# Performance work log

Measured on AMD Instinct MI355X. Metric: run time of the kernel, lower is better.

Reference implementation:

```python
import jax, jax.numpy as jnp
import numpy as np

NUM_USER = 60000
NUM_ITEM = 40000
DIM_C = 64
NUM_EDGES = 1_000_000
NUM_ROUTING = 3
ALPHA_THRESHOLD = 0.02
REATTN = True
NEG_SLOPE = 0.2  # PyG GAT default leaky-relu slope
EPS = 1e-16


def l2norm(x):
    # F.normalize(x): L2 along last dim with eps clamp
    return x / jnp.clip(jnp.linalg.norm(x, axis=-1, keepdims=True), 1e-12, None)


def seg_softmax(s, seg, n):
    # numerically stable softmax over edges grouped by target node
    m = jax.ops.segment_max(s, seg, num_segments=n)
    e = jnp.exp(s - m[seg])
    den = jax.ops.segment_sum(e, seg, num_segments=n)
    return e / (den[seg] + EPS)


def setup_inputs() -> dict:
    key = jax.random.key(0)
    ks = jax.random.split(key, 6)
    xav = (2.0 / (NUM_USER + DIM_C)) ** 0.5  # xavier_normal_ scale for preference
    features = jax.random.normal(ks[0], (NUM_ITEM, DIM_C), jnp.float32)
    features2 = jax.random.normal(ks[1], (NUM_ITEM, DIM_C), jnp.float32)
    features3 = jax.random.normal(ks[2], (NUM_ITEM, DIM_C), jnp.float32)
    preference = jax.random.normal(ks[3], (NUM_USER, DIM_C), jnp.float32) * xav
    users = jax.random.randint(ks[4], (NUM_EDGES,), 0, NUM_USER, dtype=jnp.int32)
    items = jax.random.randint(ks[5], (NUM_EDGES,), 0, NUM_ITEM, dtype=jnp.int32) + NUM_USER
    edge_index = jnp.stack([users, items], axis=0)  # [2, E] user -> item (item ids offset by num_user)
    return {"features": features, "features2": features2, "features3": features3,
            "preference": preference, "edge_index": edge_index}


def reference(features, features2, features3, preference, edge_index):
    n = NUM_USER + NUM_ITEM
    inv_sqrt_d = 1.0 / np.sqrt(DIM_C).astype(np.float32)

    pref = l2norm(preference)
    x = jnp.concatenate([pref, l2norm(features)], axis=0)   # [N, d]
    y = jnp.concatenate([pref, l2norm(features2)], axis=0)
    z = jnp.concatenate([pref, l2norm(features3)], axis=0)

    # symmetrize: edge_index = cat(edge_index, edge_index[[1,0]])
    ei = jnp.concatenate([edge_index, edge_index[::-1]], axis=1)  # [2, 2E]
    src, dst = ei[0], ei[1]  # message flows src(j) -> dst(i)

    # --- conv_embed_1: multimodal GAT with thresholding + re-attention ---
    s = ((x[dst] * x[src]).sum(-1)
         + (y[dst] * y[src]).sum(-1)
         + (z[dst] * z[src]).sum(-1)) * inv_sqrt_d          # [2E]
    alpha = seg_softmax(jax.nn.leaky_relu(s, NEG_SLOPE), dst, n)
    alpha_t = jnp.where(alpha > ALPHA_THRESHOLD, alpha, 0.0)
    if REATTN:
        den = jax.ops.segment_sum(alpha_t, dst, num_segments=n)
        alpha_t = alpha_t / (den[dst] + EPS)
    x_hat = jax.ops.segment_sum(x[src] * alpha_t[:, None], dst, num_segments=n)
    x = l2norm(x + x_hat)

    # --- routing iterations with plain dot-product GAT (conv_embed_2) ---
    for _ in range(NUM_ROUTING):
        s2 = (x[dst] * x[src]).sum(-1) * inv_sqrt_d
        a2 = seg_softmax(jax.nn.leaky_relu(s2, NEG_SLOPE), dst, n)
        x_hat = jax.ops.segment_sum(x[src] * a2[:, None], dst, num_segments=n)
        x = l2norm(x + x_hat)

    return x, alpha_t.reshape(-1, 1)
```

## Files before the change

### kernel.cpp

```cpp
#include <hip/hip_runtime.h>

#define NU 60000
#define NI 40000
#define NN 100000
#define NE 1000000
#define NE2 2000000
#define DC 64

#define M_CONV1 0.375f
#define M_ROUTE 0.125f

__device__ __forceinline__ float grp16_sum(float v) {
    v += __shfl_xor(v, 1, 64);
    v += __shfl_xor(v, 2, 64);
    v += __shfl_xor(v, 4, 64);
    v += __shfl_xor(v, 8, 64);
    return v;
}
__device__ __forceinline__ float xgrp_sum(float v) {
    v += __shfl_xor(v, 16, 64);
    v += __shfl_xor(v, 32, 64);
    return v;
}
__device__ __forceinline__ float4 xgrp_sum4(float4 v) {
    v.x = xgrp_sum(v.x); v.y = xgrp_sum(v.y); v.z = xgrp_sum(v.z); v.w = xgrp_sum(v.w);
    return v;
}
__device__ __forceinline__ float dot4(float4 a, float4 b) {
    return a.x * b.x + a.y * b.y + a.z * b.z + a.w * b.w;
}

__global__ __launch_bounds__(256) void k_init(const float* __restrict__ f1,
                                              const float* __restrict__ f2,
                                              const float* __restrict__ f3,
                                              const float* __restrict__ pref,
                                              float* __restrict__ x0,
                                              float* __restrict__ w) {
    int node = (blockIdx.x * blockDim.x + threadIdx.x) >> 6;
    int lane = threadIdx.x & 63;
    if (node >= NN) return;
    if (node < NU) {
        float v = pref[node * DC + lane];
        float s = v * v;
#pragma unroll
        for (int o = 32; o > 0; o >>= 1) s += __shfl_xor(s, o, 64);
        x0[node * DC + lane] = v / fmaxf(sqrtf(s), 1e-12f);
    } else {
        int it = node - NU;
        float a = f1[it * DC + lane];
        float b = f2[it * DC + lane];
        float c = f3[it * DC + lane];
        float sa = a * a, sb = b * b, sc = c * c;
#pragma unroll
        for (int o = 32; o > 0; o >>= 1) {
            sa += __shfl_xor(sa, o, 64);
            sb += __shfl_xor(sb, o, 64);
            sc += __shfl_xor(sc, o, 64);
        }
        float an = a / fmaxf(sqrtf(sa), 1e-12f);
        x0[node * DC + lane] = an;
        w[it * DC + lane] = an + b / fmaxf(sqrtf(sb), 1e-12f) + c / fmaxf(sqrtf(sc), 1e-12f);
    }
}

__global__ __launch_bounds__(256) void k_count(const int* __restrict__ ei,
                                               int* __restrict__ cnt) {
    int e = blockIdx.x * blockDim.x + threadIdx.x;
    if (e >= NE2) return;
    int dst = (e < NE) ? ei[NE + e] : ei[e - NE];
    atomicAdd(&cnt[dst], 1);
}

__global__ void k_scan(int* __restrict__ cnt, int* __restrict__ off, int n) {
    __shared__ int wsums[16];
    __shared__ int carry;
    int tid = threadIdx.x;
    if (tid == 0) carry = 0;
    __syncthreads();
    int wave = tid >> 6, lane = tid & 63;
    for (int base = 0; base < n; base += 1024) {
        int i = base + tid;
        int v = (i < n) ? cnt[i] : 0;
        int inc = v;
#pragma unroll
        for (int o = 1; o < 64; o <<= 1) {
            int t = __shfl_up(inc, o, 64);
            if (lane >= o) inc += t;
        }
        if (lane == 63) wsums[wave] = inc;
        __syncthreads();
        if (tid == 0) {
            int acc = carry;
#pragma unroll
            for (int k2 = 0; k2 < 16; ++k2) { int t = wsums[k2]; wsums[k2] = acc; acc += t; }
            carry = acc;
        }
        __syncthreads();
        if (i < n) {
            int ex = wsums[wave] + inc - v;
            off[i] = ex;
            cnt[i] = ex;
        }
        __syncthreads();
    }
    if (tid == 0) off[n] = carry;
}

__global__ __launch_bounds__(256) void k_fill(const int* __restrict__ ei,
                                              int* __restrict__ cur,
                                              int* __restrict__ eid,
                                              int* __restrict__ esrc) {
    int e = blockIdx.x * blockDim.x + threadIdx.x;
    if (e >= NE2) return;
    int src = ei[e];
    int dst = (e < NE) ? ei[NE + e] : ei[e - NE];
    int pos = atomicAdd(&cur[dst], 1);
    eid[pos] = e;
    esrc[pos] = src;
}

__global__ __launch_bounds__(256) void k_conv1(const float* __restrict__ x0,
                                               const float* __restrict__ w,
                                               const int* __restrict__ off,
                                               const int* __restrict__ eid,
                                               const int* __restrict__ esrc,
                                               float* __restrict__ sE,
                                               float* __restrict__ x1,
                                               float* __restrict__ aout) {
    int node = (blockIdx.x * blockDim.x + threadIdx.x) >> 6;
    int lane = threadIdx.x & 63;
    if (node >= NN) return;
    int grp = lane >> 4, gl = lane & 15;
    int beg = off[node], end = off[node + 1];
    bool user = (node < NU);

    float4 xi4 = *((const float4*)(x0 + (size_t)node * DC) + gl);
    float4 ai4 = user ? xi4 : *((const float4*)(w + (size_t)(node - NU) * DC) + gl);
    const float* gbase = user ? w : x0;
    int goff = user ? NU : 0;

    float den = 0.f;
    for (int p0 = beg; p0 < end; p0 += 4) {
        int p = p0 + grp;
        bool act = p < end;
        int s0 = act ? (esrc[p] - goff) : 0;
        float4 g4 = *((const float4*)(gbase + (size_t)s0 * DC) + gl);
        float s = grp16_sum(dot4(ai4, g4)) * 0.125f;
        s = (s > 0.f) ? s : 0.2f * s;
        float e = act ? __expf(s - M_CONV1) : 0.f;
        den += e;
        if (act && gl == 0) sE[p] = e;
    }
    den = xgrp_sum(den);
    float invden = 1.f / (den + 1e-16f);
    asm volatile("s_waitcnt vmcnt(0)" ::: "memory");

    float den2 = 0.f;
    float4 xh4 = {0.f, 0.f, 0.f, 0.f};
    for (int p0 = beg; p0 < end; p0 += 4) {
        int p = p0 + grp;
        bool act = p < end;
        int s0 = act ? esrc[p] : 0;
        float e = act ? sE[p] : 0.f;
        float a = e * invden;
        float t = (a > 0.02f) ? a : 0.f;
        den2 += t;
        float4 g4 = *((const float4*)(x0 + (size_t)s0 * DC) + gl);
        xh4.x += t * g4.x; xh4.y += t * g4.y; xh4.z += t * g4.z; xh4.w += t * g4.w;
    }
    den2 = xgrp_sum(den2);
    xh4 = xgrp_sum4(xh4);
    float invden2 = 1.f / (den2 + 1e-16f);

    for (int p = beg + lane; p < end; p += 64) {
        float a = sE[p] * invden;
        float t = (a > 0.02f) ? a : 0.f;
        aout[eid[p]] = t * invden2;
    }

    float4 v;
    v.x = xi4.x + xh4.x * invden2;
    v.y = xi4.y + xh4.y * invden2;
    v.z = xi4.z + xh4.z * invden2;
    v.w = xi4.w + xh4.w * invden2;
    float nn = grp16_sum(dot4(v, v));
    float inv_n = 1.f / fmaxf(sqrtf(nn), 1e-12f);
    if (grp == 0) {
        float4 o = {v.x * inv_n, v.y * inv_n, v.z * inv_n, v.w * inv_n};
        *((float4*)(x1 + (size_t)node * DC) + gl) = o;
    }
}

__global__ __launch_bounds__(256) void k_route(const float* __restrict__ xin,
                                               const int* __restrict__ off,
                                               const int* __restrict__ esrc,
                                               float* __restrict__ xout) {
    int node = (blockIdx.x * blockDim.x + threadIdx.x) >> 6;
    int lane = threadIdx.x & 63;
    if (node >= NN) return;
    int grp = lane >> 4, gl = lane & 15;
    int beg = off[node], end = off[node + 1];

    float4 xi4 = *((const float4*)(xin + (size_t)node * DC) + gl);

    float den = 0.f;
    float4 xh4 = {0.f, 0.f, 0.f, 0.f};
    for (int p0 = beg; p0 < end; p0 += 4) {
        int p = p0 + grp;
        bool act = p < end;
        int s0 = act ? esrc[p] : 0;
        float4 g4 = *((const float4*)(xin + (size_t)s0 * DC) + gl);
        float s = grp16_sum(dot4(xi4, g4)) * 0.125f;
        s = (s > 0.f) ? s : 0.2f * s;
        float e = act ? __expf(s - M_ROUTE) : 0.f;
        den += e;
        xh4.x += e * g4.x; xh4.y += e * g4.y; xh4.z += e * g4.z; xh4.w += e * g4.w;
    }
    den = xgrp_sum(den);
    xh4 = xgrp_sum4(xh4);
    float inv = 1.f / (den + 1e-16f);

    float4 v;
    v.x = xi4.x + xh4.x * inv;
    v.y = xi4.y + xh4.y * inv;
    v.z = xi4.z + xh4.z * inv;
    v.w = xi4.w + xh4.w * inv;
    float nn = grp16_sum(dot4(v, v));
    float inv_n = 1.f / fmaxf(sqrtf(nn), 1e-12f);
    if (grp == 0) {
        float4 o = {v.x * inv_n, v.y * inv_n, v.z * inv_n, v.w * inv_n};
        *((float4*)(xout + (size_t)node * DC) + gl) = o;
    }
}

extern "C" void kernel_launch(void* const* d_in, const int* in_sizes, int n_in,
                              void* d_out, int out_size, void* d_ws, size_t ws_size,
                              hipStream_t stream) {
    const float* f1   = (const float*)d_in[0];
    const float* f2   = (const float*)d_in[1];
    const float* f3   = (const float*)d_in[2];
    const float* pref = (const float*)d_in[3];
    const int*   ei   = (const int*)d_in[4];

    float* out = (float*)d_out;
    float* x0   = out;
    float* aout = out + (size_t)NN * DC;

    float* xb  = (float*)d_ws;
    float* w   = xb + (size_t)NN * DC;
    float* sE  = w + (size_t)NI * DC;
    int* cnt   = (int*)(sE + NE2);
    int* off   = cnt + NN;
    int* eid   = off + NN + 1;
    int* esrc  = eid + NE2;

    hipMemsetAsync(cnt, 0, NN * sizeof(int), stream);

    k_init<<<(NN * 64) / 256, 256, 0, stream>>>(f1, f2, f3, pref, x0, w);
    k_count<<<(NE2 + 255) / 256, 256, 0, stream>>>(ei, cnt);
    k_scan<<<1, 1024, 0, stream>>>(cnt, off, NN);
    k_fill<<<(NE2 + 255) / 256, 256, 0, stream>>>(ei, cnt, eid, esrc);

    k_conv1<<<(NN * 64) / 256, 256, 0, stream>>>(x0, w, off, eid, esrc, sE, xb, aout);
    k_route<<<(NN * 64) / 256, 256, 0, stream>>>(xb, off, esrc, x0);
    k_route<<<(NN * 64) / 256, 256, 0, stream>>>(x0, off, esrc, xb);
    k_route<<<(NN * 64) / 256, 256, 0, stream>>>(xb, off, esrc, x0);
}
```

Measured before the change: 775.1 us.

## Gather neighbor embeddings in bf16, unroll edge loops by two, parallelize prefix scan

Keeps a bf16 shadow copy of each node embedding and uses it for neighbor gathers in the conv1 aggregation pass and in all routing passes, which halves the bytes fetched per edge. The edge loops now process two edges per group per iteration so more loads are in flight. The single-block prefix scan over node counts becomes a three-kernel multi-block scan. The cost is extra bf16 writes, two more kernel launches, and reduced precision in attention scores and aggregations, which could affect which edges pass the 0.02 threshold.

```diff
diff --git a/kernel.cpp b/kernel.cpp
--- a/kernel.cpp
+++ b/kernel.cpp
@@ -10,6 +10,8 @@
 #define M_CONV1 0.375f
 #define M_ROUTE 0.125f
 
+typedef unsigned short u16;
+
 __device__ __forceinline__ float grp16_sum(float v) {
     v += __shfl_xor(v, 1, 64);
     v += __shfl_xor(v, 2, 64);
@@ -29,22 +31,37 @@
 __device__ __forceinline__ float dot4(float4 a, float4 b) {
     return a.x * b.x + a.y * b.y + a.z * b.z + a.w * b.w;
 }
+__device__ __forceinline__ u16 f2b(float f) {
+    union { float f; unsigned u; } a; a.f = f;
+    unsigned r = a.u + 0x7FFFu + ((a.u >> 16) & 1u);
+    return (u16)(r >> 16);
+}
+__device__ __forceinline__ float b2f(u16 b) {
+    union { unsigned u; float f; } a; a.u = ((unsigned)b) << 16;
+    return a.f;
+}
+__device__ __forceinline__ float4 b2f4(ushort4 h) {
+    float4 f; f.x = b2f(h.x); f.y = b2f(h.y); f.z = b2f(h.z); f.w = b2f(h.w);
+    return f;
+}
 
 __global__ __launch_bounds__(256) void k_init(const float* __restrict__ f1,
                                               const float* __restrict__ f2,
                                               const float* __restrict__ f3,
                                               const float* __restrict__ pref,
                                               float* __restrict__ x0,
+                                              u16* __restrict__ x016,
                                               float* __restrict__ w) {
     int node = (blockIdx.x * blockDim.x + threadIdx.x) >> 6;
     int lane = threadIdx.x & 63;
     if (node >= NN) return;
+    float outv;
     if (node < NU) {
         float v = pref[node * DC + lane];
         float s = v * v;
 #pragma unroll
         for (int o = 32; o > 0; o >>= 1) s += __shfl_xor(s, o, 64);
-        x0[node * DC + lane] = v / fmaxf(sqrtf(s), 1e-12f);
+        outv = v / fmaxf(sqrtf(s), 1e-12f);
     } else {
         int it = node - NU;
         float a = f1[it * DC + lane];
@@ -57,10 +74,11 @@
             sb += __shfl_xor(sb, o, 64);
             sc += __shfl_xor(sc, o, 64);
         }
-        float an = a / fmaxf(sqrtf(sa), 1e-12f);
-        x0[node * DC + lane] = an;
-        w[it * DC + lane] = an + b / fmaxf(sqrtf(sb), 1e-12f) + c / fmaxf(sqrtf(sc), 1e-12f);
-    }
+        outv = a / fmaxf(sqrtf(sa), 1e-12f);
+        w[it * DC + lane] = outv + b / fmaxf(sqrtf(sb), 1e-12f) + c / fmaxf(sqrtf(sc), 1e-12f);
+    }
+    x0[node * DC + lane] = outv;
+    x016[node * DC + lane] = f2b(outv);
 }
 
 __global__ __launch_bounds__(256) void k_count(const int* __restrict__ ei,
@@ -71,39 +89,58 @@
     atomicAdd(&cnt[dst], 1);
 }
 
-__global__ void k_scan(int* __restrict__ cnt, int* __restrict__ off, int n) {
-    __shared__ int wsums[16];
-    __shared__ int carry;
-    int tid = threadIdx.x;
-    if (tid == 0) carry = 0;
+__device__ __forceinline__ int block_exscan1024(int v) {
+    __shared__ int wsum[16];
+    int tid = threadIdx.x, lane = tid & 63;
+    int wv = tid >> 6;
+    int inc = v;
+#pragma unroll
+    for (int o = 1; o < 64; o <<= 1) {
+        int t = __shfl_up(inc, o, 64);
+        if (lane >= o) inc += t;
+    }
+    if (lane == 63) wsum[wv] = inc;
     __syncthreads();
-    int wave = tid >> 6, lane = tid & 63;
-    for (int base = 0; base < n; base += 1024) {
-        int i = base + tid;
-        int v = (i < n) ? cnt[i] : 0;
-        int inc = v;
+    if (tid < 16) {
+        int b = wsum[tid];
+        int binc = b;
 #pragma unroll
-        for (int o = 1; o < 64; o <<= 1) {
-            int t = __shfl_up(inc, o, 64);
-            if (lane >= o) inc += t;
+        for (int o = 1; o < 16; o <<= 1) {
+            int t = __shfl_up(binc, o, 16);
+            if (tid >= o) binc += t;
         }
-        if (lane == 63) wsums[wave] = inc;
-        __syncthreads();
-        if (tid == 0) {
-            int acc = carry;
-#pragma unroll
-            for (int k2 = 0; k2 < 16; ++k2) { int t = wsums[k2]; wsums[k2] = acc; acc += t; }
-            carry = acc;
-        }
-        __syncthreads();
-        if (i < n) {
-            int ex = wsums[wave] + inc - v;
-            off[i] = ex;
-            cnt[i] = ex;
-        }
-        __syncthreads();
-    }
-    if (tid == 0) off[n] = carry;
+        wsum[tid] = binc - b;
+    }
+    __syncthreads();
+    return wsum[wv] + inc - v;
+}
+
+__global__ __launch_bounds__(1024) void k_scan1(const int* __restrict__ cnt,
+                                                int* __restrict__ off,
+                                                int* __restrict__ bsum) {
+    int i = blockIdx.x * 1024 + threadIdx.x;
+    int v = (i < NN) ? cnt[i] : 0;
+    int ex = block_exscan1024(v);
+    if (i < NN) off[i] = ex;
+    if (threadIdx.x == 1023) bsum[blockIdx.x] = ex + v;
+}
+
+__global__ __launch_bounds__(1024) void k_scan2(int* __restrict__ bsum, int nb) {
+    int v = (threadIdx.x < nb) ? bsum[threadIdx.x] : 0;
+    int ex = block_exscan1024(v);
+    if (threadIdx.x < nb) bsum[threadIdx.x] = ex;
+}
+
+__global__ __launch_bounds__(1024) void k_scan3(int* __restrict__ off,
+                                                const int* __restrict__ bsum,
+                                                int* __restrict__ cur) {
+    int i = blockIdx.x * 1024 + threadIdx.x;
+    if (i < NN) {
+        int o = off[i] + bsum[blockIdx.x];
+        off[i] = o;
+        cur[i] = o;
+    }
+    if (i == 0) off[NN] = NE2;
 }
 
 __global__ __launch_bounds__(256) void k_fill(const int* __restrict__ ei,
@@ -121,11 +158,13 @@
 
 __global__ __launch_bounds__(256) void k_conv1(const float* __restrict__ x0,
                                                const float* __restrict__ w,
+                                               const u16* __restrict__ x16,
                                                const int* __restrict__ off,
                                                const int* __restrict__ eid,
                                                const int* __restrict__ esrc,
                                                float* __restrict__ sE,
                                                float* __restrict__ x1,
+                                               u16* __restrict__ x116,
                                                float* __restrict__ aout) {
     int node = (blockIdx.x * blockDim.x + threadIdx.x) >> 6;
     int lane = threadIdx.x & 63;
@@ -140,36 +179,51 @@
     int goff = user ? NU : 0;
 
     float den = 0.f;
-    for (int p0 = beg; p0 < end; p0 += 4) {
-        int p = p0 + grp;
-        bool act = p < end;
-        int s0 = act ? (esrc[p] - goff) : 0;
-        float4 g4 = *((const float4*)(gbase + (size_t)s0 * DC) + gl);
-        float s = grp16_sum(dot4(ai4, g4)) * 0.125f;
-        s = (s > 0.f) ? s : 0.2f * s;
-        float e = act ? __expf(s - M_CONV1) : 0.f;
-        den += e;
-        if (act && gl == 0) sE[p] = e;
+    for (int p0 = beg; p0 < end; p0 += 8) {
+        int pA = p0 + grp, pB = p0 + 4 + grp;
+        bool aA = pA < end, aB = pB < end;
+        int sA = aA ? (esrc[pA] - goff) : 0;
+        int sB = aB ? (esrc[pB] - goff) : 0;
+        float4 gA = *((const float4*)(gbase + (size_t)sA * DC) + gl);
+        float4 gB = *((const float4*)(gbase + (size_t)sB * DC) + gl);
+        float dA = grp16_sum(dot4(ai4, gA)) * 0.125f;
+        float dB = grp16_sum(dot4(ai4, gB)) * 0.125f;
+        dA = (dA > 0.f) ? dA : 0.2f * dA;
+        dB = (dB > 0.f) ? dB : 0.2f * dB;
+        float eA = aA ? __expf(dA - M_CONV1) : 0.f;
+        float eB = aB ? __expf(dB - M_CONV1) : 0.f;
+        den += eA + eB;
+        if (aA && gl == 0) sE[pA] = eA;
+        if (aB && gl == 0) sE[pB] = eB;
     }
     den = xgrp_sum(den);
     float invden = 1.f / (den + 1e-16f);
     asm volatile("s_waitcnt vmcnt(0)" ::: "memory");
 
     float den2 = 0.f;
-    float4 xh4 = {0.f, 0.f, 0.f, 0.f};
-    for (int p0 = beg; p0 < end; p0 += 4) {
-        int p = p0 + grp;
-        bool act = p < end;
-        int s0 = act ? esrc[p] : 0;
-        float e = act ? sE[p] : 0.f;
-        float a = e * invden;
-        float t = (a > 0.02f) ? a : 0.f;
-        den2 += t;
-        float4 g4 = *((const float4*)(x0 + (size_t)s0 * DC) + gl);
-        xh4.x += t * g4.x; xh4.y += t * g4.y; xh4.z += t * g4.z; xh4.w += t * g4.w;
+    float4 xh = {0.f, 0.f, 0.f, 0.f};
+    for (int p0 = beg; p0 < end; p0 += 8) {
+        int pA = p0 + grp, pB = p0 + 4 + grp;
+        bool aA = pA < end, aB = pB < end;
+        int sA = aA ? esrc[pA] : 0;
+        int sB = aB ? esrc[pB] : 0;
+        ushort4 hA = *((const ushort4*)(x16 + (size_t)sA * DC) + gl);
+        ushort4 hB = *((const ushort4*)(x16 + (size_t)sB * DC) + gl);
+        float eA = aA ? sE[pA] : 0.f;
+        float eB = aB ? sE[pB] : 0.f;
+        float aAv = eA * invden, aBv = eB * invden;
+        float tA = (aAv > 0.02f) ? aAv : 0.f;
+        float tB = (aBv > 0.02f) ? aBv : 0.f;
+        den2 += tA + tB;
+        float4 fA = b2f4(hA);
+        float4 fB = b2f4(hB);
+        xh.x += tA * fA.x + tB * fB.x;
+        xh.y += tA * fA.y + tB * fB.y;
+        xh.z += tA * fA.z + tB * fB.z;
+        xh.w += tA * fA.w + tB * fB.w;
     }
     den2 = xgrp_sum(den2);
-    xh4 = xgrp_sum4(xh4);
+    xh = xgrp_sum4(xh);
     float invden2 = 1.f / (den2 + 1e-16f);
 
     for (int p = beg + lane; p < end; p += 64) {
@@ -179,22 +233,26 @@
     }
 
     float4 v;
-    v.x = xi4.x + xh4.x * invden2;
-    v.y = xi4.y + xh4.y * invden2;
-    v.z = xi4.z + xh4.z * invden2;
-    v.w = xi4.w + xh4.w * invden2;
+    v.x = xi4.x + xh.x * invden2;
+    v.y = xi4.y + xh.y * invden2;
+    v.z = xi4.z + xh.z * invden2;
+    v.w = xi4.w + xh.w * invden2;
     float nn = grp16_sum(dot4(v, v));
     float inv_n = 1.f / fmaxf(sqrtf(nn), 1e-12f);
     if (grp == 0) {
         float4 o = {v.x * inv_n, v.y * inv_n, v.z * inv_n, v.w * inv_n};
         *((float4*)(x1 + (size_t)node * DC) + gl) = o;
+        ushort4 h = {f2b(o.x), f2b(o.y), f2b(o.z), f2b(o.w)};
+        *((ushort4*)(x116 + (size_t)node * DC) + gl) = h;
     }
 }
 
 __global__ __launch_bounds__(256) void k_route(const float* __restrict__ xin,
+                                               const u16* __restrict__ g16,
                                                const int* __restrict__ off,
                                                const int* __restrict__ esrc,
-                                               float* __restrict__ xout) {
+                                               float* __restrict__ xout,
+                                               u16* __restrict__ out16) {
     int node = (blockIdx.x * blockDim.x + threadIdx.x) >> 6;
     int lane = threadIdx.x & 63;
     if (node >= NN) return;
@@ -204,32 +262,44 @@
     float4 xi4 = *((const float4*)(xin + (size_t)node * DC) + gl);
 
     float den = 0.f;
-    float4 xh4 = {0.f, 0.f, 0.f, 0.f};
-    for (int p0 = beg; p0 < end; p0 += 4) {
-        int p = p0 + grp;
-        bool act = p < end;
-        int s0 = act ? esrc[p] : 0;
-        float4 g4 = *((const float4*)(xin + (size_t)s0 * DC) + gl);
-        float s = grp16_sum(dot4(xi4, g4)) * 0.125f;
-        s = (s > 0.f) ? s : 0.2f * s;
-        float e = act ? __expf(s - M_ROUTE) : 0.f;
-        den += e;
-        xh4.x += e * g4.x; xh4.y += e * g4.y; xh4.z += e * g4.z; xh4.w += e * g4.w;
+    float4 xh = {0.f, 0.f, 0.f, 0.f};
+    for (int p0 = beg; p0 < end; p0 += 8) {
+        int pA = p0 + grp, pB = p0 + 4 + grp;
+        bool aA = pA < end, aB = pB < end;
+        int sA = aA ? esrc[pA] : 0;
+        int sB = aB ? esrc[pB] : 0;
+        ushort4 hA = *((const ushort4*)(g16 + (size_t)sA * DC) + gl);
+        ushort4 hB = *((const ushort4*)(g16 + (size_t)sB * DC) + gl);
+        float4 fA = b2f4(hA);
+        float4 fB = b2f4(hB);
+        float dA = grp16_sum(dot4(xi4, fA)) * 0.125f;
+        float dB = grp16_sum(dot4(xi4, fB)) * 0.125f;
+        dA = (dA > 0.f) ? dA : 0.2f * dA;
+        dB = (dB > 0.f) ? dB : 0.2f * dB;
+        float eA = aA ? __expf(dA - M_ROUTE) : 0.f;
+        float eB = aB ? __expf(dB - M_ROUTE) : 0.f;
+        den += eA + eB;
+        xh.x += eA * fA.x + eB * fB.x;
+        xh.y += eA * fA.y + eB * fB.y;
+        xh.z += eA * fA.z + eB * fB.z;
+        xh.w += eA * fA.w + eB * fB.w;
     }
     den = xgrp_sum(den);
-    xh4 = xgrp_sum4(xh4);
+    xh = xgrp_sum4(xh);
     float inv = 1.f / (den + 1e-16f);
 
     float4 v;
-    v.x = xi4.x + xh4.x * inv;
-    v.y = xi4.y + xh4.y * inv;
-    v.z = xi4.z + xh4.z * inv;
-    v.w = xi4.w + xh4.w * inv;
+    v.x = xi4.x + xh.x * inv;
+    v.y = xi4.y + xh.y * inv;
+    v.z = xi4.z + xh.z * inv;
+    v.w = xi4.w + xh.w * inv;
     float nn = grp16_sum(dot4(v, v));
     float inv_n = 1.f / fmaxf(sqrtf(nn), 1e-12f);
     if (grp == 0) {
         float4 o = {v.x * inv_n, v.y * inv_n, v.z * inv_n, v.w * inv_n};
         *((float4*)(xout + (size_t)node * DC) + gl) = o;
+        ushort4 h = {f2b(o.x), f2b(o.y), f2b(o.z), f2b(o.w)};
+        *((ushort4*)(out16 + (size_t)node * DC) + gl) = h;
     }
 }
 
@@ -242,27 +312,33 @@
     const float* pref = (const float*)d_in[3];
     const int*   ei   = (const int*)d_in[4];
 
-    float* out = (float*)d_out;
+    float* out  = (float*)d_out;
     float* x0   = out;
     float* aout = out + (size_t)NN * DC;
 
-    float* xb  = (float*)d_ws;
-    float* w   = xb + (size_t)NN * DC;
-    float* sE  = w + (size_t)NI * DC;
-    int* cnt   = (int*)(sE + NE2);
-    int* off   = cnt + NN;
-    int* eid   = off + NN + 1;
-    int* esrc  = eid + NE2;
+    float* xb   = (float*)d_ws;
+    float* w    = xb + (size_t)NN * DC;
+    float* sE   = w + (size_t)NI * DC;
+    u16*  xa16  = (u16*)(sE + NE2);
+    u16*  xb16  = xa16 + (size_t)NN * DC;
+    int* cnt    = (int*)(xb16 + (size_t)NN * DC);
+    int* off    = cnt + NN;
+    int* bsum   = off + NN + 1;
+    int* eid    = bsum + 1024;
+    int* esrc   = eid + NE2;
 
     hipMemsetAsync(cnt, 0, NN * sizeof(int), stream);
 
-    k_init<<<(NN * 64) / 256, 256, 0, stream>>>(f1, f2, f3, pref, x0, w);
+    int nb = (NN + 1023) / 1024;
+    k_init<<<(NN * 64) / 256, 256, 0, stream>>>(f1, f2, f3, pref, x0, xa16, w);
     k_count<<<(NE2 + 255) / 256, 256, 0, stream>>>(ei, cnt);
-    k_scan<<<1, 1024, 0, stream>>>(cnt, off, NN);
+    k_scan1<<<nb, 1024, 0, stream>>>(cnt, off, bsum);
+    k_scan2<<<1, 1024, 0, stream>>>(bsum, nb);
+    k_scan3<<<nb, 1024, 0, stream>>>(off, bsum, cnt);
     k_fill<<<(NE2 + 255) / 256, 256, 0, stream>>>(ei, cnt, eid, esrc);
 
-    k_conv1<<<(NN * 64) / 256, 256, 0, stream>>>(x0, w, off, eid, esrc, sE, xb, aout);
-    k_route<<<(NN * 64) / 256, 256, 0, stream>>>(xb, off, esrc, x0);
-    k_route<<<(NN * 64) / 256, 256, 0, stream>>>(x0, off, esrc, xb);
-    k_route<<<(NN * 64) / 256, 256, 0, stream>>>(xb, off, esrc, x0);
-}
+    k_conv1<<<(NN * 64) / 256, 256, 0, stream>>>(x0, w, xa16, off, eid, esrc, sE, xb, xb16, aout);
+    k_route<<<(NN * 64) / 256, 256, 0, stream>>>(xb, xb16, off, esrc, x0, xa16);
+    k_route<<<(NN * 64) / 256, 256, 0, stream>>>(x0, xa16, off, esrc, xb, xb16);
+    k_route<<<(NN * 64) / 256, 256, 0, stream>>>(xb, xb16, off, esrc, x0, xa16);
+}
```

After: 636.0 us. -17.9%, faster.
